# Optimization experiments

Hardware: AMD Instinct MI355X
Metric: run time of the kernel (lower is better)

## Reference

```python
import jax, jax.numpy as jnp
import numpy as np

DT = 1.0 / 120.0  # hard-coded in the original SystemModel / EKF
N_TRAJ, T = 2048, 512
COV = np.array([2.5e-07, 2.5e-07, 0.0091, 2e-10, 1e-07, 0.01, 0.1], dtype=np.float32)


def _dynamics(s, friction, damping):
    # 6-dim puck state: [x, y, dx, dy, theta, dtheta]
    # Table damping (linear drag) + friction (smoothed Coulomb) act on linear velocity,
    # matching the SystemModel(tableDamping, tableFriction, dt=1/120) free-motion step.
    x, y, dx, dy, th, dth = s
    dx2 = dx - DT * (damping * dx + friction * jnp.tanh(100.0 * dx))
    dy2 = dy - DT * (damping * dy + friction * jnp.tanh(100.0 * dy))
    return jnp.stack([x + DT * dx, y + DT * dy, dx2, dy2, th + DT * dth, dth])


def _ekf_losses(measurements, init_state, dyna_params, Q, R, P0):
    friction, damping = dyna_params[0], dyna_params[1]
    dt_ = measurements.dtype
    H = jnp.zeros((3, 6), dt_).at[0, 0].set(1.0).at[1, 1].set(1.0).at[2, 4].set(1.0)
    I6 = jnp.eye(6, dtype=dt_)
    f = lambda s: _dynamics(s, friction, damping)
    Jf = jax.jacfwd(f)

    def step(carry, z):
        s, P = carry
        # --- predict ---
        s_pred = f(s)
        F = Jf(s)                      # 6x6 Jacobian of dynamics
        P_pred = F @ P @ F.T + Q
        # --- update ---
        y = z - H @ s_pred             # 3-dim innovation
        S = H @ P_pred @ H.T + R       # 3x3 innovation covariance
        S_inv = jnp.linalg.inv(S)
        K = P_pred @ H.T @ S_inv       # 6x3 Kalman gain
        s_new = s_pred + K @ y
        P_new = (I6 - K @ H) @ P_pred
        # per-point loss: det(S) (via slogdet as in the original) + Mahalanobis term
        sign, logdet = jnp.linalg.slogdet(S)
        loss = sign * jnp.exp(logdet) + y @ S_inv @ y
        return (s_new, P_new), loss

    def run(z_seq, s0):
        _, losses = jax.lax.scan(step, (s0, P0), z_seq)
        return losses

    return jax.vmap(run)(measurements, init_state).reshape(-1)


def setup_inputs() -> dict:
    key = jax.random.key(0)
    k1, k2 = jax.random.split(key, 2)
    measurements = jax.random.normal(k1, (N_TRAJ, T, 3), dtype=jnp.float32)
    init_state = jax.random.normal(k2, (N_TRAJ, 6), dtype=jnp.float32)
    # dyna_params = [tableFriction, tableDamping, restitution, rimFriction]
    dyna_params = jnp.array([0.1, 0.3, 0.8, 0.1], dtype=jnp.float32)
    cov = jnp.asarray(COV)
    R = jnp.diag(cov[:3])
    Q = jnp.diag(jnp.array([cov[3], cov[3], cov[4], cov[4], cov[5], cov[6]], dtype=jnp.float32))
    P0 = jnp.eye(6, dtype=jnp.float32) * 0.01
    return {"measurements": measurements, "init_state": init_state,
            "dyna_params": dyna_params, "Q": Q, "R": R, "P0": P0}


def reference(measurements, init_state, dyna_params, Q, R, P0):
    return _ekf_losses(measurements, init_state, dyna_params, Q, R, P0)
```

## Files before the change

### kernel.cpp

```cpp
#include <hip/hip_runtime.h>
#include <math.h>


#define TRIPLES 21
#define TILE    32
#define SMS4    17

__device__ __forceinline__ float frcp(float x) { return __builtin_amdgcn_rcpf(x); }

__global__ __launch_bounds__(64, 1) void ekf_kernel(
    const float* __restrict__ meas,
    const float* __restrict__ init_state,
    const float* __restrict__ dyna,
    const float* __restrict__ Qm,
    const float* __restrict__ Rm,
    const float* __restrict__ P0m,
    float* __restrict__ out,
    int n_traj, int T)
{
    __shared__ float4 sSM4[72 * SMS4];

    const int lane  = threadIdx.x;
    const int k     = lane / 3;
    const int j     = lane - 3 * k;
    const int traj0 = blockIdx.x * TRIPLES;
    const int kk    = (k < TRIPLES) ? k : (TRIPLES - 1);
    const int traj  = traj0 + kk;
    const int traj_eff = (traj < n_traj) ? traj : (n_traj - 1);

    const int NT = T / TILE;
    const int T3 = 3 * T;

    const float DTc = 1.0f / 120.0f;
    const float Cc  = 288.53900817779268f;
    const float invCc2 = 1.0f / (Cc * Cc);
    const float fric = dyna[0], damp = dyna[1];
    const bool  lin = (j == 2);
    const float ca  = lin ? 1.0f : (1.0f - DTc * damp);
    const float cf  = lin ? 0.0f : (DTc * fric);
    const float cb  = 100.0f * cf;
    const float m4cb  = -4.0f * cb;
    const float cf2Cc = 2.0f * (cf * Cc);
    const float mcfCc = -(cf * Cc);
    const int pi = (j == 0) ? 0 : (j == 1) ? 1 : 4;
    const int vi = lin ? 5 : (pi + 2);
    const float qp = Qm[pi * 7], qv = Qm[vi * 7], qc = Qm[pi * 6 + vi];
    const float r   = Rm[j * 4];
    const float nr2 = -r * r;
    const float w0  = r + r + qp;
    float p02 = P0m[pi * 6 + vi], p22 = P0m[vi * 7];
    float w   = P0m[pi * 7] + qp + r;
    float posC = Cc * init_state[traj_eff * 6 + pi];
    float xv   = Cc * init_state[traj_eff * 6 + vi];

    const int fh = lane >> 4;
    const int tw = lane & 15;
    const int fb0 = (3 * fh) * SMS4 + tw;
    float* const obase = out + (size_t)(traj0 + fh) * T + 2 * tw;

    const float* __restrict__ zlane = meas + (size_t)traj_eff * T3 + j;

    float zA[TILE], zB[TILE];
    #pragma unroll
    for (int tl = 0; tl < TILE; ++tl) zA[tl] = zlane[3 * tl];

#define EKF_PHASE(ZC, ZN, TIDX)                                              \
    do {                                                                     \
        const int tile_ = (TIDX);                                            \
        const int nt_   = (tile_ + 1 < NT) ? (tile_ + 1) : tile_;            \
        const float* __restrict__ znp_ = zlane + 96 * nt_;                   \
        _Pragma("unroll")                                                    \
        for (int tl = 0; tl < TILE; ++tl) ZN[tl] = znp_[3 * tl];             \
        float Sv[TILE], Mv[TILE];                                            \
        _Pragma("unroll")                                                    \
        for (int tl = 0; tl < TILE; ++tl) {                                  \
            const float z    = ZC[tl];                                       \
            const float e    = exp2f(xv);                    \
            const float ie   = frcp(e + 1.0f);                               \
            const float t    = fmaf(-ie, ie, ie);             \
            const float a    = fmaf(m4cb, t, ca);                            \
            const float u    = fmaf(DTc, p22, p02);                          \
            const float wp   = fmaf(DTc, p02, w);                            \
            const float S    = fmaf(DTc, u, wp);             \
            const float rs   = frcp(S);                                      \
            const float spC  = fmaf(DTc, xv, posC);                          \
            const float yvC  = fmaf(Cc, z, -spC);                            \
            const float rsyC = rs * yvC;                                     \
            const float pp02 = fmaf(a, u, qc);                               \
            const float ap   = a * p22;                                      \
            const float pp22 = fmaf(ap, a, qv);                              \
            const float sviC = fmaf(ca, xv, mcfCc);                          \
            const float svC  = fmaf(cf2Cc, ie, sviC);                        \
            xv   = fmaf(pp02, rsyC, svC);                                    \
            const float pp00 = S - r;                                        \
            posC = fmaf(pp00, rsyC, spC);                                    \
            w    = fmaf(nr2, rs, w0);                                        \
            const float k1 = pp02 * rs;                                      \
            p02 = r * k1;                                                    \
            p22 = fmaf(-k1, pp02, pp22);                                     \
            Sv[tl] = S;                                                      \
            Mv[tl] = yvC * rsyC;        \
        }                                                                    \
                       \
        _Pragma("unroll")                                                    \
        for (int h = 0; h < TILE / 2; ++h)                                   \
            sSM4[lane * SMS4 + h] =                                          \
                make_float4(Sv[2*h], Mv[2*h], Sv[2*h+1], Mv[2*h+1]);         \
                      \
        const int tb_ = tile_ * TILE;                                        \
        _Pragma("unroll")                                                    \
        for (int rr = 0; rr < 6; ++rr) {                                     \
            const int ck_ = 4 * rr + fh;                                     \
            const bool ok_ = (ck_ < TRIPLES) && (traj0 + ck_ < n_traj);      \
            const float4 a0_ = sSM4[fb0 + 204 * rr];                         \
            const float4 a1_ = sSM4[fb0 + 204 * rr + SMS4];                  \
            const float4 a2_ = sSM4[fb0 + 204 * rr + 2 * SMS4];              \
            const float l0_ = fmaf(a0_.y + a1_.y + a2_.y, invCc2,            \
                                   (a0_.x * a1_.x) * a2_.x);                 \
            const float l1_ = fmaf(a0_.w + a1_.w + a2_.w, invCc2,            \
                                   (a0_.z * a1_.z) * a2_.z);                 \
            if (ok_) *(float2*)(obase + tb_ + rr * (4 * T)) =                \
                make_float2(l0_, l1_);                                       \
        }                                                                    \
    } while (0)

    #pragma unroll 1
    for (int th = 0; th < NT; th += 2) {
        EKF_PHASE(zA, zB, th);
        if (th + 1 < NT) EKF_PHASE(zB, zA, th + 1);
    }

#undef EKF_PHASE
}

extern "C" void kernel_launch(void* const* d_in, const int* in_sizes, int n_in,
                              void* d_out, int out_size, void* d_ws, size_t ws_size,
                              hipStream_t stream) {
    const float* meas = (const float*)d_in[0];
    const float* init_state = (const float*)d_in[1];
    const float* dyna = (const float*)d_in[2];
    const float* Qm  = (const float*)d_in[3];
    const float* Rm  = (const float*)d_in[4];
    const float* P0m = (const float*)d_in[5];
    float* out = (float*)d_out;

    const int n_traj = in_sizes[1] / 6;
    const int T = in_sizes[0] / (n_traj * 3);

    const int grid = (n_traj + TRIPLES - 1) / TRIPLES;
    ekf_kernel<<<grid, 64, 0, stream>>>(meas, init_state, dyna, Qm, Rm, P0m,
                                        out, n_traj, T);
}
```

Measured before the change: 111.9 us.

## Process two trajectory groups per lane using packed float2 arithmetic

Each lane now carries two independent trajectory recurrences (A and B groups) in v2f vectors, so FMAs can map to packed FP32 instructions and the serial dependency chain gets twice the instruction-level parallelism. The grid halves to 49 blocks, tile size drops to 16 to limit register pressure, and the shared-memory reduction is reorganised into separate S and M arrays with scalar stores. Fewer blocks than CUs reduces parallelism across the chip, but the workload is latency-bound per lane, so interleaving two chains aims to hide transcendental and FMA latency. The tail guard for odd tile counts was removed.

```diff
diff --git a/kernel.cpp b/kernel.cpp
--- a/kernel.cpp
+++ b/kernel.cpp
@@ -2,11 +2,17 @@
 #include <math.h>
 
 
+typedef float v2f __attribute__((ext_vector_type(2)));
+
 #define TRIPLES 21
-#define TILE    32
-#define SMS4    17
+#define TILE    16
+#define SMS     17
 
 __device__ __forceinline__ float frcp(float x) { return __builtin_amdgcn_rcpf(x); }
+__device__ __forceinline__ v2f vsplat(float x) { v2f r; r.x = x; r.y = x; return r; }
+__device__ __forceinline__ v2f vfma(v2f a, v2f b, v2f c) {
+    return __builtin_elementwise_fma(a, b, c);
+}
 
 __global__ __launch_bounds__(64, 1) void ekf_kernel(
     const float* __restrict__ meas,
@@ -18,15 +24,18 @@
     float* __restrict__ out,
     int n_traj, int T)
 {
-    __shared__ float4 sSM4[72 * SMS4];
+    __shared__ v2f sS[64 * SMS];
+    __shared__ v2f sM[64 * SMS];
 
     const int lane  = threadIdx.x;
     const int k     = lane / 3;
     const int j     = lane - 3 * k;
-    const int traj0 = blockIdx.x * TRIPLES;
+    const int traj0 = blockIdx.x * (2 * TRIPLES);
     const int kk    = (k < TRIPLES) ? k : (TRIPLES - 1);
-    const int traj  = traj0 + kk;
-    const int traj_eff = (traj < n_traj) ? traj : (n_traj - 1);
+    const int tAi   = traj0 + kk;
+    const int tBi   = traj0 + TRIPLES + kk;
+    const int tA    = (tAi < n_traj) ? tAi : (n_traj - 1);
+    const int tB    = (tBi < n_traj) ? tBi : (n_traj - 1);
 
     const int NT = T / TILE;
     const int T3 = 3 * T;
@@ -48,86 +57,99 @@
     const float r   = Rm[j * 4];
     const float nr2 = -r * r;
     const float w0  = r + r + qp;
-    float p02 = P0m[pi * 6 + vi], p22 = P0m[vi * 7];
-    float w   = P0m[pi * 7] + qp + r;
-    float posC = Cc * init_state[traj_eff * 6 + pi];
-    float xv   = Cc * init_state[traj_eff * 6 + vi];
+
+    v2f p02, p22, w, posC, xv;
+    p02 = vsplat(P0m[pi * 6 + vi]);
+    p22 = vsplat(P0m[vi * 7]);
+    w   = vsplat(P0m[pi * 7] + qp + r);
+    posC.x = Cc * init_state[tA * 6 + pi];
+    posC.y = Cc * init_state[tB * 6 + pi];
+    xv.x   = Cc * init_state[tA * 6 + vi];
+    xv.y   = Cc * init_state[tB * 6 + vi];
+
+    const v2f vDT  = vsplat(DTc),  vCa  = vsplat(ca),   vM4  = vsplat(m4cb);
+    const v2f vQc  = vsplat(qc),   vQv  = vsplat(qv),   vR   = vsplat(r);
+    const v2f vNr2 = vsplat(nr2),  vW0  = vsplat(w0),   vCc  = vsplat(Cc);
+    const v2f vMcf = vsplat(mcfCc), vCf2 = vsplat(cf2Cc);
 
     const int fh = lane >> 4;
     const int tw = lane & 15;
-    const int fb0 = (3 * fh) * SMS4 + tw;
-    float* const obase = out + (size_t)(traj0 + fh) * T + 2 * tw;
 
-    const float* __restrict__ zlane = meas + (size_t)traj_eff * T3 + j;
+    const float* __restrict__ zpa = meas + (size_t)tA * T3 + j;
+    const float* __restrict__ zpb = meas + (size_t)tB * T3 + j;
 
-    float zA[TILE], zB[TILE];
+    v2f zA[TILE], zB[TILE];
     #pragma unroll
-    for (int tl = 0; tl < TILE; ++tl) zA[tl] = zlane[3 * tl];
+    for (int tl = 0; tl < TILE; ++tl) {
+        zA[tl].x = zpa[3 * tl];
+        zA[tl].y = zpb[3 * tl];
+    }
 
 #define EKF_PHASE(ZC, ZN, TIDX)                                              \
     do {                                                                     \
         const int tile_ = (TIDX);                                            \
         const int nt_   = (tile_ + 1 < NT) ? (tile_ + 1) : tile_;            \
-        const float* __restrict__ znp_ = zlane + 96 * nt_;                   \
-        _Pragma("unroll")                                                    \
-        for (int tl = 0; tl < TILE; ++tl) ZN[tl] = znp_[3 * tl];             \
-        float Sv[TILE], Mv[TILE];                                            \
+        const float* __restrict__ za_ = zpa + 48 * nt_;                      \
+        const float* __restrict__ zb_ = zpb + 48 * nt_;                      \
         _Pragma("unroll")                                                    \
         for (int tl = 0; tl < TILE; ++tl) {                                  \
-            const float z    = ZC[tl];                                       \
-            const float e    = exp2f(xv);                    \
-            const float ie   = frcp(e + 1.0f);                               \
-            const float t    = fmaf(-ie, ie, ie);             \
-            const float a    = fmaf(m4cb, t, ca);                            \
-            const float u    = fmaf(DTc, p22, p02);                          \
-            const float wp   = fmaf(DTc, p02, w);                            \
-            const float S    = fmaf(DTc, u, wp);             \
-            const float rs   = frcp(S);                                      \
-            const float spC  = fmaf(DTc, xv, posC);                          \
-            const float yvC  = fmaf(Cc, z, -spC);                            \
-            const float rsyC = rs * yvC;                                     \
-            const float pp02 = fmaf(a, u, qc);                               \
-            const float ap   = a * p22;                                      \
-            const float pp22 = fmaf(ap, a, qv);                              \
-            const float sviC = fmaf(ca, xv, mcfCc);                          \
-            const float svC  = fmaf(cf2Cc, ie, sviC);                        \
-            xv   = fmaf(pp02, rsyC, svC);                                    \
-            const float pp00 = S - r;                                        \
-            posC = fmaf(pp00, rsyC, spC);                                    \
-            w    = fmaf(nr2, rs, w0);                                        \
-            const float k1 = pp02 * rs;                                      \
-            p02 = r * k1;                                                    \
-            p22 = fmaf(-k1, pp02, pp22);                                     \
-            Sv[tl] = S;                                                      \
-            Mv[tl] = yvC * rsyC;        \
+            ZN[tl].x = za_[3 * tl];                                          \
+            ZN[tl].y = zb_[3 * tl];                                          \
         }                                                                    \
-                       \
         _Pragma("unroll")                                                    \
-        for (int h = 0; h < TILE / 2; ++h)                                   \
-            sSM4[lane * SMS4 + h] =                                          \
-                make_float4(Sv[2*h], Mv[2*h], Sv[2*h+1], Mv[2*h+1]);         \
-                      \
+        for (int tl = 0; tl < TILE; ++tl) {                                  \
+            const v2f z   = ZC[tl];                                          \
+            v2f e;  e.x  = exp2f(xv.x);  e.y  = exp2f(xv.y);                 \
+            const v2f e1  = e + vsplat(1.0f);                                \
+            v2f ie; ie.x = frcp(e1.x);   ie.y = frcp(e1.y);                  \
+            const v2f t_  = vfma(-ie, ie, ie);                \
+            const v2f a   = vfma(vM4, t_, vCa);                              \
+            const v2f u   = vfma(vDT, p22, p02);                             \
+            const v2f wp  = vfma(vDT, p02, w);                               \
+            const v2f S   = vfma(vDT, u, wp);                \
+            v2f rs; rs.x = frcp(S.x);    rs.y = frcp(S.y);                   \
+            const v2f spC = vfma(vDT, xv, posC);                             \
+            const v2f yvC = vfma(vCc, z, -spC);                              \
+            const v2f rsy = rs * yvC;                                        \
+            const v2f pp02 = vfma(a, u, vQc);                                \
+            const v2f ap   = a * p22;                                        \
+            const v2f pp22 = vfma(ap, a, vQv);                               \
+            const v2f svi  = vfma(vCa, xv, vMcf);                            \
+            const v2f svC  = vfma(vCf2, ie, svi);                            \
+            xv   = vfma(pp02, rsy, svC);                                     \
+            const v2f pp00 = S - vR;                                         \
+            posC = vfma(pp00, rsy, spC);                                     \
+            w    = vfma(vNr2, rs, vW0);                                      \
+            const v2f k1 = pp02 * rs;                                        \
+            p02 = vR * k1;                                                   \
+            p22 = vfma(-k1, pp02, pp22);                                     \
+            sS[lane * SMS + tl] = S;                                         \
+            sM[lane * SMS + tl] = yvC * rsy;                 \
+        }                                                                    \
+               \
         const int tb_ = tile_ * TILE;                                        \
         _Pragma("unroll")                                                    \
         for (int rr = 0; rr < 6; ++rr) {                                     \
-            const int ck_ = 4 * rr + fh;                                     \
-            const bool ok_ = (ck_ < TRIPLES) && (traj0 + ck_ < n_traj);      \
-            const float4 a0_ = sSM4[fb0 + 204 * rr];                         \
-            const float4 a1_ = sSM4[fb0 + 204 * rr + SMS4];                  \
-            const float4 a2_ = sSM4[fb0 + 204 * rr + 2 * SMS4];              \
-            const float l0_ = fmaf(a0_.y + a1_.y + a2_.y, invCc2,            \
-                                   (a0_.x * a1_.x) * a2_.x);                 \
-            const float l1_ = fmaf(a0_.w + a1_.w + a2_.w, invCc2,            \
-                                   (a0_.z * a1_.z) * a2_.z);                 \
-            if (ok_) *(float2*)(obase + tb_ + rr * (4 * T)) =                \
-                make_float2(l0_, l1_);                                       \
+            const int ck_  = 4 * rr + fh;                                    \
+            const int ckc_ = (ck_ < TRIPLES) ? ck_ : (TRIPLES - 1);          \
+            const int rb_  = (3 * ckc_) * SMS + tw;                          \
+            const v2f S0_ = sS[rb_], S1_ = sS[rb_ + SMS], S2_ = sS[rb_ + 2 * SMS]; \
+            const v2f M0_ = sM[rb_], M1_ = sM[rb_ + SMS], M2_ = sM[rb_ + 2 * SMS]; \
+            const v2f P_  = (S0_ * S1_) * S2_;                               \
+            const v2f Ms_ = (M0_ + M1_) + M2_;                               \
+            const v2f L_  = vfma(Ms_, vsplat(invCc2), P_);                   \
+            const bool okA_ = (ck_ < TRIPLES) && (traj0 + ck_ < n_traj);     \
+            const bool okB_ = (ck_ < TRIPLES) &&                             \
+                              (traj0 + TRIPLES + ck_ < n_traj);              \
+            if (okA_) out[(size_t)(traj0 + ck_) * T + tb_ + tw] = L_.x;      \
+            if (okB_) out[(size_t)(traj0 + TRIPLES + ck_) * T + tb_ + tw] = L_.y; \
         }                                                                    \
     } while (0)
 
     #pragma unroll 1
     for (int th = 0; th < NT; th += 2) {
         EKF_PHASE(zA, zB, th);
-        if (th + 1 < NT) EKF_PHASE(zB, zA, th + 1);
+        EKF_PHASE(zB, zA, th + 1);
     }
 
 #undef EKF_PHASE
@@ -147,7 +169,7 @@
     const int n_traj = in_sizes[1] / 6;
     const int T = in_sizes[0] / (n_traj * 3);
 
-    const int grid = (n_traj + TRIPLES - 1) / TRIPLES;
+    const int grid = (n_traj + 2 * TRIPLES - 1) / (2 * TRIPLES);
     ekf_kernel<<<grid, 64, 0, stream>>>(meas, init_state, dyna, Qm, Rm, P0m,
                                         out, n_traj, T);
 }
```

Result: slower. 138.2 us (+23.5%).

## Warp-specialize: producer wave stages measurements and flushes losses for compute wave

Applied to the files above, without the earlier changes.

Splits each block into two waves: wave 0 runs the sequential EKF recurrence, and wave 1 prefetches the next measurement tile into double-buffered shared memory and reduces and writes the previous tile's losses. This takes global loads and output reduction off the serial critical path of the compute wave, at the cost of a block-wide barrier per tile and extra LDS. Per-block register pressure changes since the compute wave no longer holds two 32-float z tiles.

```diff
diff --git a/kernel.cpp b/kernel.cpp
--- a/kernel.cpp
+++ b/kernel.cpp
@@ -8,7 +8,7 @@
 
 __device__ __forceinline__ float frcp(float x) { return __builtin_amdgcn_rcpf(x); }
 
-__global__ __launch_bounds__(64, 1) void ekf_kernel(
+__global__ __launch_bounds__(128, 1) void ekf_kernel(
     const float* __restrict__ meas,
     const float* __restrict__ init_state,
     const float* __restrict__ dyna,
@@ -18,9 +18,12 @@
     float* __restrict__ out,
     int n_traj, int T)
 {
-    __shared__ float4 sSM4[72 * SMS4];
+    __shared__ float4 zs4[2][TILE / 4][64];
+    __shared__ float4 sSM4[2][72 * SMS4];
 
-    const int lane  = threadIdx.x;
+    const int tid   = threadIdx.x;
+    const int wid   = tid >> 6;
+    const int lane  = tid & 63;
     const int k     = lane / 3;
     const int j     = lane - 3 * k;
     const int traj0 = blockIdx.x * TRIPLES;
@@ -57,64 +60,26 @@
     const int tw = lane & 15;
     const int fb0 = (3 * fh) * SMS4 + tw;
     float* const obase = out + (size_t)(traj0 + fh) * T + 2 * tw;
-
     const float* __restrict__ zlane = meas + (size_t)traj_eff * T3 + j;
 
-    float zA[TILE], zB[TILE];
-    #pragma unroll
-    for (int tl = 0; tl < TILE; ++tl) zA[tl] = zlane[3 * tl];
+#define STAGE(TIDX, BUF)                                                     \
+    do {                                                                     \
+        const float* __restrict__ zp_ = zlane + 96 * (TIDX);                 \
+        _Pragma("unroll")                                                    \
+        for (int tt = 0; tt < TILE; ++tt)                                    \
+            ((float*)&zs4[BUF][tt >> 2][lane])[tt & 3] = zp_[3 * tt];        \
+    } while (0)
 
-#define EKF_PHASE(ZC, ZN, TIDX)                                              \
+#define FLUSH(TIDX, BUF)                                                     \
     do {                                                                     \
-        const int tile_ = (TIDX);                                            \
-        const int nt_   = (tile_ + 1 < NT) ? (tile_ + 1) : tile_;            \
-        const float* __restrict__ znp_ = zlane + 96 * nt_;                   \
-        _Pragma("unroll")                                                    \
-        for (int tl = 0; tl < TILE; ++tl) ZN[tl] = znp_[3 * tl];             \
-        float Sv[TILE], Mv[TILE];                                            \
-        _Pragma("unroll")                                                    \
-        for (int tl = 0; tl < TILE; ++tl) {                                  \
-            const float z    = ZC[tl];                                       \
-            const float e    = exp2f(xv);                    \
-            const float ie   = frcp(e + 1.0f);                               \
-            const float t    = fmaf(-ie, ie, ie);             \
-            const float a    = fmaf(m4cb, t, ca);                            \
-            const float u    = fmaf(DTc, p22, p02);                          \
-            const float wp   = fmaf(DTc, p02, w);                            \
-            const float S    = fmaf(DTc, u, wp);             \
-            const float rs   = frcp(S);                                      \
-            const float spC  = fmaf(DTc, xv, posC);                          \
-            const float yvC  = fmaf(Cc, z, -spC);                            \
-            const float rsyC = rs * yvC;                                     \
-            const float pp02 = fmaf(a, u, qc);                               \
-            const float ap   = a * p22;                                      \
-            const float pp22 = fmaf(ap, a, qv);                              \
-            const float sviC = fmaf(ca, xv, mcfCc);                          \
-            const float svC  = fmaf(cf2Cc, ie, sviC);                        \
-            xv   = fmaf(pp02, rsyC, svC);                                    \
-            const float pp00 = S - r;                                        \
-            posC = fmaf(pp00, rsyC, spC);                                    \
-            w    = fmaf(nr2, rs, w0);                                        \
-            const float k1 = pp02 * rs;                                      \
-            p02 = r * k1;                                                    \
-            p22 = fmaf(-k1, pp02, pp22);                                     \
-            Sv[tl] = S;                                                      \
-            Mv[tl] = yvC * rsyC;        \
-        }                                                                    \
-                       \
-        _Pragma("unroll")                                                    \
-        for (int h = 0; h < TILE / 2; ++h)                                   \
-            sSM4[lane * SMS4 + h] =                                          \
-                make_float4(Sv[2*h], Mv[2*h], Sv[2*h+1], Mv[2*h+1]);         \
-                      \
-        const int tb_ = tile_ * TILE;                                        \
+        const int tb_ = (TIDX) * TILE;                                       \
         _Pragma("unroll")                                                    \
         for (int rr = 0; rr < 6; ++rr) {                                     \
             const int ck_ = 4 * rr + fh;                                     \
             const bool ok_ = (ck_ < TRIPLES) && (traj0 + ck_ < n_traj);      \
-            const float4 a0_ = sSM4[fb0 + 204 * rr];                         \
-            const float4 a1_ = sSM4[fb0 + 204 * rr + SMS4];                  \
-            const float4 a2_ = sSM4[fb0 + 204 * rr + 2 * SMS4];              \
+            const float4 a0_ = sSM4[BUF][fb0 + 204 * rr];                    \
+            const float4 a1_ = sSM4[BUF][fb0 + 204 * rr + SMS4];             \
+            const float4 a2_ = sSM4[BUF][fb0 + 204 * rr + 2 * SMS4];         \
             const float l0_ = fmaf(a0_.y + a1_.y + a2_.y, invCc2,            \
                                    (a0_.x * a1_.x) * a2_.x);                 \
             const float l1_ = fmaf(a0_.w + a1_.w + a2_.w, invCc2,            \
@@ -124,13 +89,68 @@
         }                                                                    \
     } while (0)
 
+#define STEP(ZZ, TL)                                                         \
+    do {                                                                     \
+        const float z    = (ZZ);                                             \
+        const float e    = exp2f(xv);                        \
+        const float ie   = frcp(e + 1.0f);                                   \
+        const float t    = fmaf(-ie, ie, ie);                 \
+        const float a    = fmaf(m4cb, t, ca);                                \
+        const float u    = fmaf(DTc, p22, p02);                              \
+        const float wp   = fmaf(DTc, p02, w);                                \
+        const float S    = fmaf(DTc, u, wp);                 \
+        const float rs   = frcp(S);                                          \
+        const float spC  = fmaf(DTc, xv, posC);                              \
+        const float yvC  = fmaf(Cc, z, -spC);                                \
+        const float rsyC = rs * yvC;                                         \
+        const float pp02 = fmaf(a, u, qc);                                   \
+        const float ap   = a * p22;                                          \
+        const float pp22 = fmaf(ap, a, qv);                                  \
+        const float sviC = fmaf(ca, xv, mcfCc);                              \
+        const float svC  = fmaf(cf2Cc, ie, sviC);                            \
+        xv   = fmaf(pp02, rsyC, svC);                                        \
+        const float pp00 = S - r;                                            \
+        posC = fmaf(pp00, rsyC, spC);                                        \
+        w    = fmaf(nr2, rs, w0);                                            \
+        const float k1 = pp02 * rs;                                          \
+        p02 = r * k1;                                                        \
+        p22 = fmaf(-k1, pp02, pp22);                                         \
+        Sv[TL] = S;                                                          \
+        Mv[TL] = yvC * rsyC;                                                 \
+    } while (0)
+
+    int cur = 0;
+    if (wid == 1) STAGE(0, 0);
+    __syncthreads();
+
     #pragma unroll 1
-    for (int th = 0; th < NT; th += 2) {
-        EKF_PHASE(zA, zB, th);
-        if (th + 1 < NT) EKF_PHASE(zB, zA, th + 1);
+    for (int tile = 0; tile < NT; ++tile) {
+        if (wid == 0) {
+            float Sv[TILE], Mv[TILE];
+            #pragma unroll
+            for (int q = 0; q < TILE / 4; ++q) {
+                const float4 zq = zs4[cur][q][lane];
+                STEP(zq.x, 4 * q + 0);
+                STEP(zq.y, 4 * q + 1);
+                STEP(zq.z, 4 * q + 2);
+                STEP(zq.w, 4 * q + 3);
+            }
+            #pragma unroll
+            for (int h = 0; h < TILE / 2; ++h)
+                sSM4[cur][lane * SMS4 + h] =
+                    make_float4(Sv[2*h], Mv[2*h], Sv[2*h+1], Mv[2*h+1]);
+        } else {
+            if (tile + 1 < NT) STAGE(tile + 1, cur ^ 1);
+            if (tile > 0)      FLUSH(tile - 1, cur ^ 1);
+        }
+        __syncthreads();
+        cur ^= 1;
     }
+    if (wid == 1) FLUSH(NT - 1, cur ^ 1);
 
-#undef EKF_PHASE
+#undef STEP
+#undef FLUSH
+#undef STAGE
 }
 
 extern "C" void kernel_launch(void* const* d_in, const int* in_sizes, int n_in,
@@ -148,6 +168,6 @@
     const int T = in_sizes[0] / (n_traj * 3);
 
     const int grid = (n_traj + TRIPLES - 1) / TRIPLES;
-    ekf_kernel<<<grid, 64, 0, stream>>>(meas, init_state, dyna, Qm, Rm, P0m,
-                                        out, n_traj, T);
+    ekf_kernel<<<grid, 128, 0, stream>>>(meas, init_state, dyna, Qm, Rm, P0m,
+                                         out, n_traj, T);
 }
```

After: 104.2 us. -6.9%, faster.
